# Performance work log

Hardware: AMD Instinct MI355X
Metric: run time of the kernel (lower is better)

Reference implementation:

```python
import jax, jax.numpy as jnp
import numpy as np

N_EMBD = 1024
N_HEAD = 16
B, T = 2, 2048
LN_EPS = 1e-5


def _linear_params(key, d_in, d_out):
    k1, k2 = jax.random.split(key)
    bound = 1.0 / np.sqrt(d_in)
    W = jax.random.uniform(k1, (d_in, d_out), jnp.float32, -bound, bound)
    b = jax.random.uniform(k2, (d_out,), jnp.float32, -bound, bound)
    return W, b


def setup_inputs() -> dict:
    key = jax.random.key(0)
    ks = jax.random.split(key, 8)
    x = jax.random.normal(ks[0], (B, T, N_EMBD), jnp.float32)
    Wq, bq = _linear_params(ks[1], N_EMBD, N_EMBD)
    Wk, bk = _linear_params(ks[2], N_EMBD, N_EMBD)
    Wv, bv = _linear_params(ks[3], N_EMBD, N_EMBD)
    Wo, bo = _linear_params(ks[4], N_EMBD, N_EMBD)
    W1, b1 = _linear_params(ks[5], N_EMBD, 4 * N_EMBD)
    W2, b2 = _linear_params(ks[6], 4 * N_EMBD, N_EMBD)
    ln1_g = jnp.ones((N_EMBD,), jnp.float32)
    ln1_b = jnp.zeros((N_EMBD,), jnp.float32)
    ln2_g = jnp.ones((N_EMBD,), jnp.float32)
    ln2_b = jnp.zeros((N_EMBD,), jnp.float32)
    return dict(x=x, Wq=Wq, bq=bq, Wk=Wk, bk=bk, Wv=Wv, bv=bv, Wo=Wo, bo=bo,
                W1=W1, b1=b1, W2=W2, b2=b2,
                ln1_g=ln1_g, ln1_b=ln1_b, ln2_g=ln2_g, ln2_b=ln2_b)


def _layernorm(x, g, b):
    mu = jnp.mean(x, axis=-1, keepdims=True)
    var = jnp.mean(jnp.square(x - mu), axis=-1, keepdims=True)
    return (x - mu) * jax.lax.rsqrt(var + LN_EPS) * g + b


def _attention(x, Wq, bq, Wk, bk, Wv, bv, Wo, bo):
    Bsz, Tlen, C = x.shape
    hd = C // N_HEAD
    q = (x @ Wq + bq).reshape(Bsz, Tlen, N_HEAD, hd)
    k = (x @ Wk + bk).reshape(Bsz, Tlen, N_HEAD, hd)
    v = (x @ Wv + bv).reshape(Bsz, Tlen, N_HEAD, hd)
    scale = 1.0 / np.sqrt(hd)
    # NOTE: the original module's mask buffer is all ones -> masked_fill is a
    # no-op, so attention is FULL (non-causal) despite the class name.
    att = jnp.einsum('bqhd,bkhd->bhqk', q, k) * scale
    att = jax.nn.softmax(att, axis=-1)
    y = jnp.einsum('bhqk,bkhd->bqhd', att, v).reshape(Bsz, Tlen, C)
    return y @ Wo + bo


def reference(x, Wq, bq, Wk, bk, Wv, bv, Wo, bo, W1, b1, W2, b2,
              ln1_g, ln1_b, ln2_g, ln2_b):
    x = x + _attention(_layernorm(x, ln1_g, ln1_b), Wq, bq, Wk, bk, Wv, bv, Wo, bo)
    h = _layernorm(x, ln2_g, ln2_b)
    h = jax.nn.gelu(h @ W1 + b1, approximate=False) @ W2 + b2
    return x + h
```

## Files before the change

### kernel.cpp

```cpp
#include <hip/hip_runtime.h>
#include <hip/hip_bf16.h>
#include <math.h>


typedef __bf16 bf16x8 __attribute__((ext_vector_type(8)));
typedef float f32x4 __attribute__((ext_vector_type(4)));

__device__ __forceinline__ unsigned short f2bf(float f) {
  union { float f; unsigned int u; } v; v.f = f;
  unsigned int u = v.u;
  unsigned int r = (u + 0x7fffu + ((u >> 16) & 1u)) >> 16;
  return (unsigned short)r;
}

__device__ __forceinline__ unsigned int fbits(float f) {
  union { float f; unsigned int u; } v; v.f = f;
  return v.u;
}

__device__ __forceinline__ bf16x8 ld_bf16x8(const unsigned short* p) {
  union { uint4 u; bf16x8 v; } x;
  x.u = *(const uint4*)p;
  return x.v;
}

__device__ __forceinline__ float fast_exp2(float x) {
#if __has_builtin(__builtin_amdgcn_exp2f)
  return __builtin_amdgcn_exp2f(x);
#else
  return exp2f(x);
#endif
}

__device__ __forceinline__ size_t ckidx(int row, int col, int Kd) {
  return ((size_t)(row >> 4) * (Kd >> 5) + (col >> 5)) * 512 +
         (size_t)(((col >> 3) & 3) * 128 + (row & 15) * 8 + (col & 7));
}

__device__ __forceinline__ void async_copy16(const void* g, void* l) {
  __builtin_amdgcn_global_load_lds(
      (const __attribute__((address_space(1))) void*)g,
      (__attribute__((address_space(3))) void*)l, 16, 0, 0);
}

__global__ __launch_bounds__(256) void prep_kernel(
    const float* __restrict__ Wq, const float* __restrict__ Wk,
    const float* __restrict__ Wv, const float* __restrict__ Wo,
    const float* __restrict__ W1, const float* __restrict__ W2,
    unsigned short* __restrict__ WqT, unsigned short* __restrict__ WkT,
    unsigned short* __restrict__ WvT, unsigned short* __restrict__ WoT,
    unsigned short* __restrict__ W1T, unsigned short* __restrict__ W2T,
    const float* __restrict__ x, const float* __restrict__ g,
    const float* __restrict__ b, unsigned short* __restrict__ xn) {
  __shared__ unsigned short tile[32][33];
  __shared__ float red[8];
  const int id = blockIdx.x;
  const int t = threadIdx.x;

  if (id < 12288) {
    const float* W;
    unsigned short* Wt;
    int N, K, bx, by;
    if (id < 4096) {
      const int wsel = id >> 10, b10 = id & 1023;
      W = wsel == 0 ? Wq : (wsel == 1 ? Wk : (wsel == 2 ? Wv : Wo));
      Wt = wsel == 0 ? WqT : (wsel == 1 ? WkT : (wsel == 2 ? WvT : WoT));
      N = 1024; K = 1024; bx = b10 & 31; by = b10 >> 5;
    } else if (id < 8192) {
      const int b12 = id - 4096;
      W = W1; Wt = W1T; N = 4096; K = 1024; bx = b12 & 127; by = b12 >> 7;
    } else {
      const int b12 = id - 8192;
      W = W2; Wt = W2T; N = 1024; K = 4096; bx = b12 & 31; by = b12 >> 5;
    }
    const int n0 = bx * 32, k0 = by * 32;
    const int r = t >> 3, cq = (t & 7) * 4;
    float4 v = *(const float4*)&W[(size_t)(k0 + r) * N + n0 + cq];
    tile[cq + 0][r] = f2bf(v.x);
    tile[cq + 1][r] = f2bf(v.y);
    tile[cq + 2][r] = f2bf(v.z);
    tile[cq + 3][r] = f2bf(v.w);
    __syncthreads();
    ushort4 o;
    o.x = tile[r][cq + 0];
    o.y = tile[r][cq + 1];
    o.z = tile[r][cq + 2];
    o.w = tile[r][cq + 3];
    *(ushort4*)&Wt[ckidx(n0 + r, k0 + cq, K)] = o;
  } else {
    const int row = id - 12288;
    const float4 v = ((const float4*)(x + (size_t)row * 1024))[t];
    float s = v.x + v.y + v.z + v.w;
    float s2 = v.x * v.x + v.y * v.y + v.z * v.z + v.w * v.w;
    for (int o = 32; o > 0; o >>= 1) {
      s += __shfl_xor(s, o, 64);
      s2 += __shfl_xor(s2, o, 64);
    }
    const int w = t >> 6;
    if ((t & 63) == 0) { red[w] = s; red[4 + w] = s2; }
    __syncthreads();
    s = red[0] + red[1] + red[2] + red[3];
    s2 = red[4] + red[5] + red[6] + red[7];
    const float mu = s * (1.f / 1024.f);
    const float var = s2 * (1.f / 1024.f) - mu * mu;
    const float rs = rsqrtf(var + 1e-5f);
    const float4 gg = ((const float4*)g)[t];
    const float4 bb = ((const float4*)b)[t];
    ushort4 o4;
    o4.x = f2bf((v.x - mu) * rs * gg.x + bb.x);
    o4.y = f2bf((v.y - mu) * rs * gg.y + bb.y);
    o4.z = f2bf((v.z - mu) * rs * gg.z + bb.z);
    o4.w = f2bf((v.w - mu) * rs * gg.w + bb.w);
    *(ushort4*)&xn[ckidx(row, t * 4, 1024)] = o4;
  }
}

__global__ __launch_bounds__(256) void ln_kernel(
    const float* __restrict__ x, const float* __restrict__ g,
    const float* __restrict__ b, unsigned short* __restrict__ out) {
  const int row = blockIdx.x, t = threadIdx.x;
  const float4 v = ((const float4*)(x + (size_t)row * 1024))[t];
  float s = v.x + v.y + v.z + v.w;
  float s2 = v.x * v.x + v.y * v.y + v.z * v.z + v.w * v.w;
  for (int o = 32; o > 0; o >>= 1) {
    s += __shfl_xor(s, o, 64);
    s2 += __shfl_xor(s2, o, 64);
  }
  __shared__ float red[8];
  const int w = t >> 6;
  if ((t & 63) == 0) { red[w] = s; red[4 + w] = s2; }
  __syncthreads();
  s = red[0] + red[1] + red[2] + red[3];
  s2 = red[4] + red[5] + red[6] + red[7];
  const float mu = s * (1.f / 1024.f);
  const float var = s2 * (1.f / 1024.f) - mu * mu;
  const float rs = rsqrtf(var + 1e-5f);
  const float4 gg = ((const float4*)g)[t];
  const float4 bb = ((const float4*)b)[t];
  ushort4 o4;
  o4.x = f2bf((v.x - mu) * rs * gg.x + bb.x);
  o4.y = f2bf((v.y - mu) * rs * gg.y + bb.y);
  o4.z = f2bf((v.z - mu) * rs * gg.z + bb.z);
  o4.w = f2bf((v.w - mu) * rs * gg.w + bb.w);
  *(ushort4*)&out[ckidx(row, t * 4, 1024)] = o4;
}

enum { MODE_QKV = 0, MODE_RES = 1, MODE_GELU = 2 };

#define QSCALE 0.18033688011112043f

template <int MODE>
__global__ __launch_bounds__(512) void gemm256_kernel(
    const unsigned short* __restrict__ A, const unsigned short* __restrict__ Bt,
    const float* __restrict__ bias0, const float* __restrict__ bias1,
    const float* __restrict__ bias2,
    void* __restrict__ out0, void* __restrict__ out1, void* __restrict__ out2,
    int M, int N, int K) {
  __shared__ __align__(16) unsigned short L[2][64 * 512];
  const int t = threadIdx.x;
  const int l = t & 63, w = t >> 6;
  const int l8 = l * 8;
  const int lr = l & 15, lq = l >> 4;

  const int NT = N >> 8;
  const int q8 = (int)gridDim.x >> 3;
  const int bid = blockIdx.x;
  const int wg = (bid & 7) * q8 + (bid >> 3);
  const int mt = wg / NT, nt = wg % NT;
  const int m0 = mt << 8, n0 = nt << 8;

  const int ag0 = (w >> 2) * 8;
  const int bg0 = (w & 3) * 4;
  const int K32 = K >> 5;

  f32x4 acc[8][4];
#pragma unroll
  for (int i = 0; i < 8; i++)
#pragma unroll
    for (int j = 0; j < 4; j++) {
      f32x4 z = {0.f, 0.f, 0.f, 0.f};
      acc[i][j] = z;
    }

  auto issue = [&](int kt, int slot) {
    const int k32 = kt * 2;
#pragma unroll
    for (int j = 0; j < 8; j++) {
      const int c = j * 8 + w;
      unsigned short* dst = &L[slot][c * 512 + l8];
      if (j < 4) {
        const size_t cid =
            (size_t)((m0 >> 4) + (c & 15)) * K32 + (k32 + (c >> 4));
        async_copy16(&A[cid * 512 + l8], dst);
      } else {
        const int cb = c - 32;
        const size_t cid =
            (size_t)((n0 >> 4) + (cb & 15)) * K32 + (k32 + (cb >> 4));
        async_copy16(&Bt[cid * 512 + l8], dst);
      }
    }
  };

  const int KT = K >> 6;
  issue(0, 0);
  for (int kt = 0; kt < KT; kt++) {
    const int slot = kt & 1;
    if (kt + 1 < KT) {
      issue(kt + 1, slot ^ 1);
      asm volatile("s_waitcnt vmcnt(8)" ::: "memory");
    } else {
      asm volatile("s_waitcnt vmcnt(0)" ::: "memory");
    }
    __builtin_amdgcn_s_barrier();

    bf16x8 bfr[2][4];
#pragma unroll
    for (int kk = 0; kk < 2; kk++)
#pragma unroll
      for (int nj = 0; nj < 4; nj++)
        bfr[kk][nj] =
            ld_bf16x8(&L[slot][(32 + kk * 16 + bg0 + nj) * 512 + l8]);

#pragma unroll
    for (int half = 0; half < 2; half++) {
#pragma unroll
      for (int kk = 0; kk < 2; kk++) {
        bf16x8 afr[4];
#pragma unroll
        for (int mi = 0; mi < 4; mi++)
          afr[mi] = ld_bf16x8(
              &L[slot][(kk * 16 + ag0 + half * 4 + mi) * 512 + l8]);
        __builtin_amdgcn_s_setprio(1);
#pragma unroll
        for (int mi = 0; mi < 4; mi++)
#pragma unroll
          for (int nj = 0; nj < 4; nj++)
            acc[half * 4 + mi][nj] = __builtin_amdgcn_mfma_f32_16x16x32_bf16(
                afr[mi], bfr[kk][nj], acc[half * 4 + mi][nj], 0, 0, 0);
        __builtin_amdgcn_s_setprio(0);
      }
    }
    __builtin_amdgcn_s_barrier();
  }

#pragma unroll
  for (int mi8 = 0; mi8 < 8; mi8++) {
#pragma unroll
    for (int nj = 0; nj < 4; nj++) {
#pragma unroll
      for (int i = 0; i < 4; i++) {
        const int gm = m0 + (w >> 2) * 128 + mi8 * 16 + lq * 4 + i;
        const int gn = n0 + (w & 3) * 64 + nj * 16 + lr;
        const float v = acc[mi8][nj][i];
        if (MODE == MODE_QKV) {
          const int sel = gn >> 10, cn = gn & 1023;
          const int hh = cn >> 6, d = cn & 63;
          const int bb2 = gm >> 11, tok = gm & 2047;
          const size_t bh = (size_t)bb2 * 16 + hh;
          float u = v + (sel == 0 ? bias0 : (sel == 1 ? bias1 : bias2))[cn];
          if (sel == 0) {
            u *= QSCALE;
            const int qt = tok >> 7, r7 = tok & 127;
            const int ww = r7 >> 5, ss = (r7 >> 4) & 1, qlr = r7 & 15;
            const int kk = d >> 5, lq2 = (d >> 3) & 3, e = d & 7;
            const size_t idx =
                (((((bh * 16 + qt) * 4 + ww) * 2 + ss) * 2 + kk) << 9) +
                (lq2 * 16 + qlr) * 8 + e;
            ((unsigned short*)out0)[idx] = f2bf(u);
          } else if (sel == 1) {
            const int ktile = tok >> 6, r6 = tok & 63;
            const int nt2 = r6 >> 4, klr = r6 & 15;
            const int kk = d >> 5, lq2 = (d >> 3) & 3, e = d & 7;
            const size_t idx =
                ((((bh * 32 + ktile) * 4 + nt2) * 2 + kk) << 9) +
                (lq2 * 16 + klr) * 8 + e;
            ((unsigned short*)out1)[idx] = f2bf(u);
          } else {
            const int ktile = tok >> 6, r6 = tok & 63;
            const int kb = r6 >> 5, lq2 = (r6 >> 3) & 3, e = r6 & 7;
            const int nt2 = d >> 4, vlr = d & 15;
            const size_t idx =
                ((((bh * 32 + ktile) * 2 + kb) * 4 + nt2) << 9) +
                (lq2 * 16 + vlr) * 8 + e;
            ((unsigned short*)out2)[idx] = f2bf(u);
          }
        } else {
          const float u = v + bias0[gn];
          const float ge = 0.5f * u * (1.f + erff(u * 0.70710678118654752f));
          ((unsigned short*)out0)[ckidx(gm, gn, N)] = f2bf(ge);
        }
      }
    }
  }
}

template <int BM, int BN, int MODE>
__global__ __launch_bounds__(256) void gemm_kernel(
    const unsigned short* __restrict__ A, const unsigned short* __restrict__ Bt,
    const float* __restrict__ bias0, const float* __restrict__ residual,
    void* __restrict__ out0, int M, int N, int K) {
  constexpr int MI = BM / 32;
  constexpr int NI = BN / 32;
  constexpr int ACH = BM / 8;
  constexpr int BCH = BN / 8;
  static_assert(ACH / 4 + BCH / 4 == 6, "vmcnt immediate assumes 6 loads");
  __shared__ __align__(16) unsigned short As[3][BM * 64];
  __shared__ __align__(16) unsigned short Bs[3][BN * 64];
  const int t = threadIdx.x;

  const int NT = N / BN;
  const int NTX = NT >> 3;
  const int bid = blockIdx.x;
  const int xcd = bid & 7, local = bid >> 3;
  const int nt_ = xcd * NTX + local % NTX;
  const int mt = local / NTX;
  const int m0 = mt * BM, n0 = nt_ * BN;

  const int l = t & 63, w = t >> 6;
  const int l8 = l * 8;
  const int lr = l & 15, lq = l >> 4;
  const int K32 = K >> 5;

  f32x4 acc[MI][NI];
#pragma unroll
  for (int i = 0; i < MI; i++)
#pragma unroll
    for (int j = 0; j < NI; j++) {
      f32x4 z = {0.f, 0.f, 0.f, 0.f};
      acc[i][j] = z;
    }

  auto issue = [&](int kt, int p) {
    const int k32 = kt * 2;
#pragma unroll
    for (int j = 0; j < ACH / 4; j++) {
      const int c = j * 4 + w;
      const int g = c % (BM / 16), kk = c / (BM / 16);
      const size_t cid = (size_t)((m0 >> 4) + g) * K32 + (k32 + kk);
      async_copy16(&A[cid * 512 + l8], &As[p][c * 512 + l8]);
    }
#pragma unroll
    for (int j = 0; j < BCH / 4; j++) {
      const int c = j * 4 + w;
      const int g = c % (BN / 16), kk = c / (BN / 16);
      const size_t cid = (size_t)((n0 >> 4) + g) * K32 + (k32 + kk);
      async_copy16(&Bt[cid * 512 + l8], &Bs[p][c * 512 + l8]);
    }
  };

  const int KT = K >> 6;
  issue(0, 0);
  issue(1, 1);
  for (int kt = 0; kt < KT; kt++) {
    const int p = kt % 3;
    if (kt + 1 < KT)
      asm volatile("s_waitcnt vmcnt(6)" ::: "memory");
    else
      asm volatile("s_waitcnt vmcnt(0)" ::: "memory");
    __builtin_amdgcn_s_barrier();
    if (kt + 2 < KT) issue(kt + 2, (kt + 2) % 3);
#pragma unroll
    for (int kk = 0; kk < 2; kk++) {
      bf16x8 af[MI], bf[NI];
#pragma unroll
      for (int mi = 0; mi < MI; mi++)
        af[mi] = ld_bf16x8(
            &As[p][(kk * (BM / 16) + (w >> 1) * (BM / 32) + mi) * 512 + l8]);
#pragma unroll
      for (int ni = 0; ni < NI; ni++)
        bf[ni] = ld_bf16x8(
            &Bs[p][(kk * (BN / 16) + (w & 1) * (BN / 32) + ni) * 512 + l8]);
      __builtin_amdgcn_s_setprio(1);
#pragma unroll
      for (int mi = 0; mi < MI; mi++)
#pragma unroll
        for (int ni = 0; ni < NI; ni++)
          acc[mi][ni] = __builtin_amdgcn_mfma_f32_16x16x32_bf16(
              af[mi], bf[ni], acc[mi][ni], 0, 0, 0);
      __builtin_amdgcn_s_setprio(0);
    }
  }

  const int wm = (w >> 1) * (BM / 2), wn = (w & 1) * (BN / 2);
#pragma unroll
  for (int mi = 0; mi < MI; mi++) {
#pragma unroll
    for (int ni = 0; ni < NI; ni++) {
#pragma unroll
      for (int i = 0; i < 4; i++) {
        const int gm = m0 + wm + mi * 16 + lq * 4 + i;
        const int gn = n0 + wn + ni * 16 + lr;
        ((float*)out0)[(size_t)gm * N + gn] =
            acc[mi][ni][i] + bias0[gn] + residual[(size_t)gm * N + gn];
      }
    }
  }
}

__global__ __launch_bounds__(256) void attn_kernel(
    const unsigned short* __restrict__ Qp, const unsigned short* __restrict__ Kp,
    const unsigned short* __restrict__ Vp, unsigned short* __restrict__ O) {
  __shared__ __align__(16) unsigned short Ps[128 * 72];
  const int id = blockIdx.x;
  const int xcd = id & 7, loc = id >> 3;
  const int bh = xcd * 4 + (loc >> 4);
  const int qt = loc & 15;
  const int t = threadIdx.x, l = t & 63, w = t >> 6;
  const int lr = l & 15, lq = l >> 4;
  const int l8 = l * 8;
  const size_t rowBase = (size_t)(bh >> 4) * 2048;
  const int col0 = (bh & 15) * 64;

  const unsigned short* Qb_ = Qp + ((((size_t)bh * 16 + qt) * 4 + w) << 11);
  bf16x8 qf[2][2];
#pragma unroll
  for (int s = 0; s < 2; s++)
#pragma unroll
    for (int kk = 0; kk < 2; kk++)
      qf[s][kk] = ld_bf16x8(&Qb_[((s * 2 + kk) << 9) + l8]);

  const unsigned short* Kb_ = Kp + ((size_t)bh << 17);
  const unsigned short* Vb_ = Vp + ((size_t)bh << 17);

  bf16x8 kf[2][4];
#pragma unroll
  for (int nt = 0; nt < 4; nt++)
#pragma unroll
    for (int kk = 0; kk < 2; kk++)
      kf[kk][nt] = ld_bf16x8(&Kb_[((nt * 2 + kk) << 9) + l8]);

  f32x4 oacc[2][4];
#pragma unroll
  for (int s = 0; s < 2; s++)
#pragma unroll
    for (int nt = 0; nt < 4; nt++) {
      f32x4 z = {0.f, 0.f, 0.f, 0.f};
      oacc[s][nt] = z;
    }
  float lp[2] = {0.f, 0.f};

  for (int kt = 0; kt < 32; kt++) {
    const unsigned short* vtile = Vb_ + ((size_t)kt << 12);
    bf16x8 vf[2][4];
#pragma unroll
    for (int kb = 0; kb < 2; kb++)
#pragma unroll
      for (int nt = 0; nt < 4; nt++)
        vf[kb][nt] = ld_bf16x8(&vtile[((kb * 4 + nt) << 9) + l8]);

    f32x4 st[2][4];
#pragma unroll
    for (int s = 0; s < 2; s++)
#pragma unroll
      for (int nt = 0; nt < 4; nt++) {
        f32x4 z = {0.f, 0.f, 0.f, 0.f};
        st[s][nt] = z;
      }
#pragma unroll
    for (int nt = 0; nt < 4; nt++) {
      __builtin_amdgcn_s_setprio(1);
      st[0][nt] = __builtin_amdgcn_mfma_f32_16x16x32_bf16(kf[0][nt], qf[0][0], st[0][nt], 0, 0, 0);
      st[1][nt] = __builtin_amdgcn_mfma_f32_16x16x32_bf16(kf[0][nt], qf[1][0], st[1][nt], 0, 0, 0);
      st[0][nt] = __builtin_amdgcn_mfma_f32_16x16x32_bf16(kf[1][nt], qf[0][1], st[0][nt], 0, 0, 0);
      st[1][nt] = __builtin_amdgcn_mfma_f32_16x16x32_bf16(kf[1][nt], qf[1][1], st[1][nt], 0, 0, 0);
      __builtin_amdgcn_s_setprio(0);
    }

    const unsigned short* ktile_p = Kb_ + ((size_t)((kt + 1) & 31) << 12);
#pragma unroll
    for (int nt = 0; nt < 4; nt++)
#pragma unroll
      for (int kk = 0; kk < 2; kk++)
        kf[kk][nt] = ld_bf16x8(&ktile_p[((nt * 2 + kk) << 9) + l8]);

#pragma unroll
    for (int s = 0; s < 2; s++) {
      float rsum = 0.f;
#pragma unroll
      for (int nt = 0; nt < 4; nt++)
#pragma unroll
        for (int i = 0; i < 4; i++) {
          const float pv = fast_exp2(st[s][nt][i]);
          st[s][nt][i] = pv;
          rsum += pv;
        }
      lp[s] += rsum;
    }

#pragma unroll
    for (int s = 0; s < 2; s++)
#pragma unroll
      for (int nt = 0; nt < 4; nt++) {
        uint2 pk;
        pk.x = __builtin_amdgcn_perm(fbits(st[s][nt][1]), fbits(st[s][nt][0]), 0x07060302u);
        pk.y = __builtin_amdgcn_perm(fbits(st[s][nt][3]), fbits(st[s][nt][2]), 0x07060302u);
        *(uint2*)&Ps[(w * 32 + s * 16 + lr) * 72 + nt * 16 + lq * 4] = pk;
      }

#pragma unroll
    for (int kb = 0; kb < 2; kb++) {
      bf16x8 pf0 = ld_bf16x8(&Ps[(w * 32 + lr) * 72 + kb * 32 + lq * 8]);
      bf16x8 pf1 = ld_bf16x8(&Ps[(w * 32 + 16 + lr) * 72 + kb * 32 + lq * 8]);
      __builtin_amdgcn_s_setprio(1);
#pragma unroll
      for (int nt = 0; nt < 4; nt++) {
        oacc[0][nt] = __builtin_amdgcn_mfma_f32_16x16x32_bf16(pf0, vf[kb][nt], oacc[0][nt], 0, 0, 0);
        oacc[1][nt] = __builtin_amdgcn_mfma_f32_16x16x32_bf16(pf1, vf[kb][nt], oacc[1][nt], 0, 0, 0);
      }
      __builtin_amdgcn_s_setprio(0);
    }
  }

#pragma unroll
  for (int s = 0; s < 2; s++) {
    float li = lp[s];
    li += __shfl_xor(li, 16, 64);
    li += __shfl_xor(li, 32, 64);
    const float inv = 1.f / li;
#pragma unroll
    for (int nt = 0; nt < 4; nt++)
#pragma unroll
      for (int i = 0; i < 4; i++) {
        const int orow = (int)rowBase + qt * 128 + w * 32 + s * 16 + lq * 4 + i;
        const int ocol = col0 + nt * 16 + lr;
        O[ckidx(orow, ocol, 1024)] = f2bf(oacc[s][nt][i] * inv);
      }
  }
}

extern "C" void kernel_launch(void* const* d_in, const int* in_sizes, int n_in,
                              void* d_out, int out_size, void* d_ws, size_t ws_size,
                              hipStream_t stream) {
  const float* x    = (const float*)d_in[0];
  const float* Wq   = (const float*)d_in[1];
  const float* bq   = (const float*)d_in[2];
  const float* Wk   = (const float*)d_in[3];
  const float* bk   = (const float*)d_in[4];
  const float* Wv   = (const float*)d_in[5];
  const float* bv   = (const float*)d_in[6];
  const float* Wo   = (const float*)d_in[7];
  const float* bo   = (const float*)d_in[8];
  const float* W1   = (const float*)d_in[9];
  const float* b1   = (const float*)d_in[10];
  const float* W2   = (const float*)d_in[11];
  const float* b2   = (const float*)d_in[12];
  const float* ln1g = (const float*)d_in[13];
  const float* ln1b = (const float*)d_in[14];
  const float* ln2g = (const float*)d_in[15];
  const float* ln2b = (const float*)d_in[16];

  char* ws = (char*)d_ws;
  const size_t MB = 1024ull * 1024ull;
  unsigned short* WqT = (unsigned short*)(ws + 0 * MB);
  unsigned short* WkT = (unsigned short*)(ws + 2 * MB);
  unsigned short* WvT = (unsigned short*)(ws + 4 * MB);
  unsigned short* WoT = (unsigned short*)(ws + 6 * MB);
  unsigned short* W1T = (unsigned short*)(ws + 8 * MB);
  unsigned short* W2T = (unsigned short*)(ws + 16 * MB);
  unsigned short* xn  = (unsigned short*)(ws + 24 * MB);
  unsigned short* Qp  = (unsigned short*)(ws + 32 * MB);
  unsigned short* Kp  = (unsigned short*)(ws + 40 * MB);
  unsigned short* Vp  = (unsigned short*)(ws + 48 * MB);
  unsigned short* Ob  = (unsigned short*)(ws + 56 * MB);
  float*          x1  = (float*)(ws + 64 * MB);
  unsigned short* h2  = (unsigned short*)(ws + 80 * MB);
  unsigned short* Hb  = (unsigned short*)(ws + 24 * MB);

  const dim3 blk(256);
  const dim3 blk512(512);

  prep_kernel<<<dim3(16384), blk, 0, stream>>>(
      Wq, Wk, Wv, Wo, W1, W2, WqT, WkT, WvT, WoT, W1T, W2T,
      x, ln1g, ln1b, xn);

  gemm256_kernel<MODE_QKV><<<dim3(192), blk512, 0, stream>>>(
      xn, WqT, bq, bk, bv, Qp, Kp, Vp, 4096, 3072, 1024);

  attn_kernel<<<dim3(512), blk, 0, stream>>>(Qp, Kp, Vp, Ob);

  gemm_kernel<64, 128, MODE_RES><<<dim3(512), blk, 0, stream>>>(
      Ob, WoT, bo, x, x1, 4096, 1024, 1024);

  ln_kernel<<<4096, blk, 0, stream>>>(x1, ln2g, ln2b, h2);

  gemm256_kernel<MODE_GELU><<<dim3(256), blk512, 0, stream>>>(
      h2, W1T, b1, nullptr, nullptr, Hb, nullptr, nullptr, 4096, 4096, 1024);

  gemm_kernel<64, 128, MODE_RES><<<dim3(512), blk, 0, stream>>>(
      Hb, W2T, b2, x1, (float*)d_out, 4096, 1024, 4096);
}
```

Baseline: 366.3 us.

## Load B operand directly from global into registers in residual GEMMs

The residual-add GEMMs (attention output projection and MLP down projection) no longer stage the weight tile through LDS. Each wave loads its B fragments straight from global memory into double-buffered registers, one k-tile ahead. Only A stays on the async LDS triple buffer, which roughly halves shared memory and removes the LDS reads for B. The cost is more register pressure and uncoalesced-style per-wave global loads of B that other waves in the block duplicate. The loop is unrolled by two, uses a masked wrap-around prefetch, and assumes KT is even and a power of two.

```diff
diff --git a/kernel.cpp b/kernel.cpp
--- a/kernel.cpp
+++ b/kernel.cpp
@@ -294,18 +294,14 @@
   }
 }
 
-template <int BM, int BN, int MODE>
-__global__ __launch_bounds__(256) void gemm_kernel(
+template <int BM, int BN>
+__global__ __launch_bounds__(256) void gemm_bdir_kernel(
     const unsigned short* __restrict__ A, const unsigned short* __restrict__ Bt,
     const float* __restrict__ bias0, const float* __restrict__ residual,
-    void* __restrict__ out0, int M, int N, int K) {
+    float* __restrict__ out0, int M, int N, int K) {
   constexpr int MI = BM / 32;
   constexpr int NI = BN / 32;
-  constexpr int ACH = BM / 8;
-  constexpr int BCH = BN / 8;
-  static_assert(ACH / 4 + BCH / 4 == 6, "vmcnt immediate assumes 6 loads");
   __shared__ __align__(16) unsigned short As[3][BM * 64];
-  __shared__ __align__(16) unsigned short Bs[3][BN * 64];
   const int t = threadIdx.x;
 
   const int NT = N / BN;
@@ -320,6 +316,11 @@
   const int l8 = l * 8;
   const int lr = l & 15, lq = l >> 4;
   const int K32 = K >> 5;
+  const int KT = K >> 6;
+  const int KM = KT - 1;
+
+  const int bg = (n0 + (w & 1) * (BN / 2)) >> 4;
+  const int ag = (w >> 1) * MI;
 
   f32x4 acc[MI][NI];
 #pragma unroll
@@ -330,55 +331,60 @@
       acc[i][j] = z;
     }
 
-  auto issue = [&](int kt, int p) {
+  auto issueA = [&](int kt, int slot) {
     const int k32 = kt * 2;
 #pragma unroll
-    for (int j = 0; j < ACH / 4; j++) {
+    for (int j = 0; j < 2; j++) {
       const int c = j * 4 + w;
-      const int g = c % (BM / 16), kk = c / (BM / 16);
+      const int g = c & (BM / 16 - 1);
+      const int kk = c / (BM / 16);
       const size_t cid = (size_t)((m0 >> 4) + g) * K32 + (k32 + kk);
-      async_copy16(&A[cid * 512 + l8], &As[p][c * 512 + l8]);
-    }
-#pragma unroll
-    for (int j = 0; j < BCH / 4; j++) {
-      const int c = j * 4 + w;
-      const int g = c % (BN / 16), kk = c / (BN / 16);
-      const size_t cid = (size_t)((n0 >> 4) + g) * K32 + (k32 + kk);
-      async_copy16(&Bt[cid * 512 + l8], &Bs[p][c * 512 + l8]);
+      async_copy16(&A[cid * 512 + l8], &As[slot][c * 512 + l8]);
     }
   };
 
-  const int KT = K >> 6;
-  issue(0, 0);
-  issue(1, 1);
-  for (int kt = 0; kt < KT; kt++) {
-    const int p = kt % 3;
-    if (kt + 1 < KT)
-      asm volatile("s_waitcnt vmcnt(6)" ::: "memory");
-    else
-      asm volatile("s_waitcnt vmcnt(0)" ::: "memory");
-    __builtin_amdgcn_s_barrier();
-    if (kt + 2 < KT) issue(kt + 2, (kt + 2) % 3);
+  auto loadB = [&](int kt, bf16x8 (&br)[2][NI]) {
+#pragma unroll
+    for (int kk = 0; kk < 2; kk++)
+#pragma unroll
+      for (int ni = 0; ni < NI; ni++) {
+        const size_t cid = (size_t)(bg + ni) * K32 + (kt * 2 + kk);
+        br[kk][ni] = ld_bf16x8(&Bt[cid * 512 + l8]);
+      }
+  };
+
+  auto compute = [&](int slot, bf16x8 (&br)[2][NI]) {
 #pragma unroll
     for (int kk = 0; kk < 2; kk++) {
-      bf16x8 af[MI], bf[NI];
+      bf16x8 af[MI];
 #pragma unroll
       for (int mi = 0; mi < MI; mi++)
         af[mi] = ld_bf16x8(
-            &As[p][(kk * (BM / 16) + (w >> 1) * (BM / 32) + mi) * 512 + l8]);
-#pragma unroll
-      for (int ni = 0; ni < NI; ni++)
-        bf[ni] = ld_bf16x8(
-            &Bs[p][(kk * (BN / 16) + (w & 1) * (BN / 32) + ni) * 512 + l8]);
+            &As[slot][((kk * (BM / 16)) + ag + mi) * 512 + l8]);
       __builtin_amdgcn_s_setprio(1);
 #pragma unroll
       for (int mi = 0; mi < MI; mi++)
 #pragma unroll
         for (int ni = 0; ni < NI; ni++)
           acc[mi][ni] = __builtin_amdgcn_mfma_f32_16x16x32_bf16(
-              af[mi], bf[ni], acc[mi][ni], 0, 0, 0);
+              af[mi], br[kk][ni], acc[mi][ni], 0, 0, 0);
       __builtin_amdgcn_s_setprio(0);
     }
+  };
+
+  bf16x8 br0[2][NI], br1[2][NI];
+  issueA(0, 0);
+  issueA(1, 1);
+  loadB(0, br0);
+  for (int kt = 0; kt < KT; kt += 2) {
+    asm volatile("s_waitcnt vmcnt(10)\n\ts_barrier" ::: "memory");
+    issueA((kt + 2) & KM, (kt + 2) % 3);
+    loadB((kt + 1) & KM, br1);
+    compute(kt % 3, br0);
+    asm volatile("s_waitcnt vmcnt(10)\n\ts_barrier" ::: "memory");
+    issueA((kt + 3) & KM, (kt + 3) % 3);
+    loadB((kt + 2) & KM, br0);
+    compute((kt + 1) % 3, br1);
   }
 
   const int wm = (w >> 1) * (BM / 2), wn = (w & 1) * (BN / 2);
@@ -390,7 +396,7 @@
       for (int i = 0; i < 4; i++) {
         const int gm = m0 + wm + mi * 16 + lq * 4 + i;
         const int gn = n0 + wn + ni * 16 + lr;
-        ((float*)out0)[(size_t)gm * N + gn] =
+        out0[(size_t)gm * N + gn] =
             acc[mi][ni][i] + bias0[gn] + residual[(size_t)gm * N + gn];
       }
     }
@@ -578,7 +584,7 @@
 
   attn_kernel<<<dim3(512), blk, 0, stream>>>(Qp, Kp, Vp, Ob);
 
-  gemm_kernel<64, 128, MODE_RES><<<dim3(512), blk, 0, stream>>>(
+  gemm_bdir_kernel<64, 128><<<dim3(512), blk, 0, stream>>>(
       Ob, WoT, bo, x, x1, 4096, 1024, 1024);
 
   ln_kernel<<<4096, blk, 0, stream>>>(x1, ln2g, ln2b, h2);
@@ -586,6 +592,6 @@
   gemm256_kernel<MODE_GELU><<<dim3(256), blk512, 0, stream>>>(
       h2, W1T, b1, nullptr, nullptr, Hb, nullptr, nullptr, 4096, 4096, 1024);
 
-  gemm_kernel<64, 128, MODE_RES><<<dim3(512), blk, 0, stream>>>(
+  gemm_bdir_kernel<64, 128><<<dim3(512), blk, 0, stream>>>(
       Hb, W2T, b2, x1, (float*)d_out, 4096, 1024, 4096);
 }
```

Measured after the change: 376.6 us. +2.8%, slower.
